# Optimization experiments

Measured on AMD Instinct MI355X. Metric: run time of the kernel, lower is better.

## Reference

```python
import jax, jax.numpy as jnp
import numpy as np

TEMPERATURE = 0.1
EPS = 1e-12  # F.normalize eps

B, D = 4096, 1024

def setup_inputs() -> dict:
    key = jax.random.key(0)
    k1, k2 = jax.random.split(key)
    return {
        "feature_view_1": jax.random.normal(k1, (B, D), dtype=jnp.float32),
        "feature_view_2": jax.random.normal(k2, (B, D), dtype=jnp.float32),
    }

def reference(feature_view_1, feature_view_2):
    b = feature_view_1.shape[0]
    n = 2 * b  # n_views = 2
    # cat views and L2-normalize each row (F.normalize semantics: x / max(||x||, eps))
    f = jnp.concatenate([feature_view_1, feature_view_2], axis=0)  # [2B, D]
    norm = jnp.maximum(jnp.linalg.norm(f, axis=1, keepdims=True), EPS)
    f = f / norm
    # similarity matrix scaled by temperature
    sim = jnp.matmul(f, f.T) / TEMPERATURE  # [2B, 2B]
    idx = jnp.arange(n)
    # positive for row i is the other view of the same sample: column (i+B) mod 2B
    pos = sim[idx, (idx + b) % n]  # [2B]
    # cross-entropy with label 0 over [pos, negatives] == lse over off-diagonal minus pos
    sim_offdiag = jnp.where(idx[:, None] == idx[None, :], -jnp.inf, sim)
    lse = jax.nn.logsumexp(sim_offdiag, axis=1)  # [2B]
    # CrossEntropyLoss default reduction: mean
    return jnp.mean(lse - pos)
```

## Files before the change

kernel.cpp:

```cpp
#include <hip/hip_runtime.h>
#include <stdint.h>

#define B_ROWS 4096
#define N_ROWS 8192
#define D_DIM  1024
#define NBLK   64
#define NTRI   2080
#define XCDQ   260

typedef __attribute__((ext_vector_type(4))) float f32x4;

static __device__ __forceinline__ void async_copy16(const unsigned char* g, unsigned char* l) {
  __builtin_amdgcn_global_load_lds(
      (const __attribute__((address_space(1))) unsigned int*)g,
      (__attribute__((address_space(3))) unsigned int*)l, 16, 0, 0);
}

static __device__ __forceinline__ void wg_barrier() {
  asm volatile("" ::: "memory");
  __builtin_amdgcn_s_barrier();
  asm volatile("" ::: "memory");
}

__global__ __launch_bounds__(256) void normalize_kernel(
    const float* __restrict__ f1, const float* __restrict__ f2,
    unsigned char* __restrict__ F8, float* __restrict__ rowsum) {
  const int row = blockIdx.x;
  const int tid = threadIdx.x;
  const float* src = (row < B_ROWS) ? (f1 + (size_t)row * D_DIM)
                                    : (f2 + (size_t)(row - B_ROWS) * D_DIM);
  float4 v = ((const float4*)src)[tid];
  float ss = v.x * v.x + v.y * v.y + v.z * v.z + v.w * v.w;
#pragma unroll
  for (int m = 1; m < 64; m <<= 1) ss += __shfl_xor(ss, m, 64);
  __shared__ float red[4];
  if ((tid & 63) == 0) red[tid >> 6] = ss;
  __syncthreads();
  ss = red[0] + red[1] + red[2] + red[3];
  const float s16 = 16.0f / fmaxf(sqrtf(ss), 1e-12f);
  int w = 0;
  w = __builtin_amdgcn_cvt_pk_fp8_f32(v.x * s16, v.y * s16, w, 0);
  w = __builtin_amdgcn_cvt_pk_fp8_f32(v.z * s16, v.w * s16, w, 1);
  ((int*)(F8 + (size_t)row * D_DIM))[tid] = w;
  if (tid == 0) rowsum[row] = 0.0f;
}

__global__ __launch_bounds__(256, 3) void simloss_kernel(
    const unsigned char* __restrict__ F8, float* __restrict__ rowsum,
    float* __restrict__ pos) {
  __shared__ __align__(16) unsigned char lA[3][128 * 64];
  __shared__ __align__(16) unsigned char lB[3][128 * 64];

  int s = (blockIdx.x & 7) * XCDQ + (blockIdx.x >> 3);
  int SJ = 0;
  for (;;) { const int c = 64 * SJ + 36; if (s < c) break; s -= c; ++SJ; }
  int SI = 0;
  while (SI < SJ && s >= 64) { s -= 64; ++SI; }
  int di, dj;
  if (SI < SJ) {
    dj = s >> 3; di = s & 7;
  } else {
    dj = 0; while (s > dj) { s -= (dj + 1); ++dj; } di = s;
  }
  const int bi = SI * 8 + di;
  const int bj = SJ * 8 + dj;

  const int tid  = threadIdx.x;
  const int lane = tid & 63;
  const int wv   = __builtin_amdgcn_readfirstlane(tid >> 6);
  const int waveRow = wv >> 1;
  const int waveCol = wv & 1;
  const int q   = lane >> 4;
  const int l16 = lane & 15;

  const int iBase = bi * 128;
  const int jBase = bj * 128;
  const unsigned char* __restrict__ GA = F8 + (size_t)iBase * D_DIM;
  const unsigned char* __restrict__ GB = F8 + (size_t)jBase * D_DIM;

  f32x4 acc[4][4];
#pragma unroll
  for (int a = 0; a < 4; ++a)
#pragma unroll
    for (int b = 0; b < 4; ++b) acc[a][b] = (f32x4){0.f, 0.f, 0.f, 0.f};

#define STAGE(BUFI, K0)                                                      \
  {                                                                          \
    _Pragma("unroll") for (int it = 0; it < 2; ++it) {                       \
      const int lc = it * 256 + tid;                                         \
      const int rr = lc >> 2;                                                \
      const int gc = (lc & 3) ^ ((rr >> 1) & 3);                             \
      const size_t goff = (size_t)rr * D_DIM + (K0) + gc * 16;               \
      async_copy16(GA + goff, &lA[BUFI][lc * 16]);                           \
    }                                                                        \
    _Pragma("unroll") for (int it = 0; it < 2; ++it) {                       \
      const int lc = it * 256 + tid;                                         \
      const int rr = lc >> 2;                                                \
      const int gc = (lc & 3) ^ ((rr >> 1) & 3);                             \
      const size_t goff = (size_t)rr * D_DIM + (K0) + gc * 16;               \
      async_copy16(GB + goff, &lB[BUFI][lc * 16]);                           \
    }                                                                        \
  }

#define STEP(BUFI)                                                           \
  {                                                                          \
    long aF[4][2], bF[4][2];                                                 \
    _Pragma("unroll") for (int mi = 0; mi < 4; ++mi) {                       \
      const int rr  = waveRow * 64 + mi * 16 + l16;                          \
      const int swz = (rr >> 1) & 3;                                         \
      const int base = rr * 64 + ((q & 1) << 3);                             \
      aF[mi][0] = *(const long*)&lA[BUFI][base + ((((q >> 1)    ) ^ swz) << 4)]; \
      aF[mi][1] = *(const long*)&lA[BUFI][base + ((((q >> 1) + 2) ^ swz) << 4)]; \
    }                                                                        \
    _Pragma("unroll") for (int ni = 0; ni < 4; ++ni) {                       \
      const int rr  = waveCol * 64 + ni * 16 + l16;                          \
      const int swz = (rr >> 1) & 3;                                         \
      const int base = rr * 64 + ((q & 1) << 3);                             \
      bF[ni][0] = *(const long*)&lB[BUFI][base + ((((q >> 1)    ) ^ swz) << 4)]; \
      bF[ni][1] = *(const long*)&lB[BUFI][base + ((((q >> 1) + 2) ^ swz) << 4)]; \
    }                                                                        \
    _Pragma("unroll") for (int mi = 0; mi < 4; ++mi)                         \
      _Pragma("unroll") for (int ni = 0; ni < 4; ++ni) {                     \
        acc[mi][ni] = __builtin_amdgcn_mfma_f32_16x16x32_fp8_fp8(            \
            aF[mi][0], bF[ni][0], acc[mi][ni], 0, 0, 0);                     \
        acc[mi][ni] = __builtin_amdgcn_mfma_f32_16x16x32_fp8_fp8(            \
            aF[mi][1], bF[ni][1], acc[mi][ni], 0, 0, 0);                     \
      }                                                                      \
  }

  STAGE(0, 0)
  STAGE(1, 64)

#pragma unroll 1
  for (int t = 0; t < 16; ++t) {
    if (t == 15) { asm volatile("s_waitcnt vmcnt(0)" ::: "memory"); }
    else         { asm volatile("s_waitcnt vmcnt(4)" ::: "memory"); }
    wg_barrier();
    if (t < 14) { STAGE((t + 2) % 3, (t + 2) * 64) }
    STEP(t % 3)
  }
#undef STEP
#undef STAGE

  const bool offdiag = (bi != bj);
  float colAcc[4] = {0.f, 0.f, 0.f, 0.f};

#pragma unroll
  for (int mi = 0; mi < 4; ++mi) {
#pragma unroll
    for (int reg = 0; reg < 4; ++reg) {
      const int i = iBase + waveRow * 64 + mi * 16 + q * 4 + reg;
      float s2 = 0.0f;
#pragma unroll
      for (int ni = 0; ni < 4; ++ni) {
        const int j = jBase + waveCol * 64 + ni * 16 + l16;
        const float sim = acc[mi][ni][reg] * (10.0f / 256.0f);
        const float e = (j == i) ? 0.0f : __expf(sim - 10.0f);
        s2 += e;
        colAcc[ni] += e;
        if (i < B_ROWS && j == i + B_ROWS) pos[i] = sim;
      }
#pragma unroll
      for (int m = 1; m < 16; m <<= 1) s2 += __shfl_xor(s2, m, 64);
      if (l16 == 0) atomicAdd(&rowsum[i], s2);
    }
  }

  if (offdiag) {
#pragma unroll
    for (int ni = 0; ni < 4; ++ni) {
      float c = colAcc[ni];
      c += __shfl_xor(c, 16, 64);
      c += __shfl_xor(c, 32, 64);
      if (q == 0) {
        const int j = jBase + waveCol * 64 + ni * 16 + l16;
        atomicAdd(&rowsum[j], c);
      }
    }
  }
}

__global__ __launch_bounds__(1024) void finalize_kernel(
    const float* __restrict__ rowsum, const float* __restrict__ pos,
    float* __restrict__ out) {
  const int tid = threadIdx.x;
  float a = 0.0f;
  for (int i = tid; i < N_ROWS; i += 1024)
    a += logf(rowsum[i]) + 10.0f - pos[i & (B_ROWS - 1)];
#pragma unroll
  for (int m = 1; m < 64; m <<= 1) a += __shfl_xor(a, m, 64);
  __shared__ float red[16];
  if ((tid & 63) == 0) red[tid >> 6] = a;
  __syncthreads();
  if (tid == 0) {
    float t = 0.0f;
#pragma unroll
    for (int w = 0; w < 16; ++w) t += red[w];
    out[0] = t * (1.0f / N_ROWS);
  }
}

extern "C" void kernel_launch(void* const* d_in, const int* in_sizes, int n_in,
                              void* d_out, int out_size, void* d_ws, size_t ws_size,
                              hipStream_t stream) {
  const float* f1 = (const float*)d_in[0];
  const float* f2 = (const float*)d_in[1];
  unsigned char* F8 = (unsigned char*)d_ws;
  float* rowsum = (float*)((char*)d_ws + (size_t)N_ROWS * D_DIM);
  float* pos    = rowsum + N_ROWS;
  float* out    = (float*)d_out;

  hipLaunchKernelGGL(normalize_kernel, dim3(N_ROWS), dim3(256), 0, stream, f1, f2, F8, rowsum);
  hipLaunchKernelGGL(simloss_kernel, dim3(NTRI), dim3(256), 0, stream, F8, rowsum, pos);
  hipLaunchKernelGGL(finalize_kernel, dim3(1), dim3(1024), 0, stream, rowsum, pos, out);
}
```

Measured before the change: 150.4 us.

## Switch FP8 GEMM to 32x32x64 scaled MFMA with matching LDS swizzle

Replaces the 16x16x32 FP8 MFMA tiling (4x4 tiles per wave, two MFMAs per k-step) with the gfx950 32x32x64 f8f6f4 scaled MFMA (2x2 tiles per wave, one MFMA per k-step) using unit scales. The LDS swizzle and fragment loads change to 16-byte vector reads per half-wave, and the epilogue is remapped to the 32x32 accumulator layout. This is meant to cut MFMA issue count and LDS read instructions, at the cost of wider shuffle reductions in the epilogue and reliance on the new layout mapping being correct.

```diff
diff --git a/kernel.cpp b/kernel.cpp
--- a/kernel.cpp
+++ b/kernel.cpp
@@ -8,7 +8,9 @@
 #define NTRI   2080
 #define XCDQ   260
 
-typedef __attribute__((ext_vector_type(4))) float f32x4;
+typedef __attribute__((ext_vector_type(4)))  int   i32x4;
+typedef __attribute__((ext_vector_type(8)))  int   i32x8;
+typedef __attribute__((ext_vector_type(16))) float f32x16;
 
 static __device__ __forceinline__ void async_copy16(const unsigned char* g, unsigned char* l) {
   __builtin_amdgcn_global_load_lds(
@@ -70,33 +72,33 @@
   const int wv   = __builtin_amdgcn_readfirstlane(tid >> 6);
   const int waveRow = wv >> 1;
   const int waveCol = wv & 1;
-  const int q   = lane >> 4;
-  const int l16 = lane & 15;
+  const int l31 = lane & 31;
+  const int h   = lane >> 5;
 
   const int iBase = bi * 128;
   const int jBase = bj * 128;
   const unsigned char* __restrict__ GA = F8 + (size_t)iBase * D_DIM;
   const unsigned char* __restrict__ GB = F8 + (size_t)jBase * D_DIM;
 
-  f32x4 acc[4][4];
-#pragma unroll
-  for (int a = 0; a < 4; ++a)
-#pragma unroll
-    for (int b = 0; b < 4; ++b) acc[a][b] = (f32x4){0.f, 0.f, 0.f, 0.f};
+  f32x16 acc[2][2];
+#pragma unroll
+  for (int a = 0; a < 2; ++a)
+#pragma unroll
+    for (int b = 0; b < 2; ++b) acc[a][b] = (f32x16)(0.0f);
 
 #define STAGE(BUFI, K0)                                                      \
   {                                                                          \
     _Pragma("unroll") for (int it = 0; it < 2; ++it) {                       \
       const int lc = it * 256 + tid;                                         \
       const int rr = lc >> 2;                                                \
-      const int gc = (lc & 3) ^ ((rr >> 1) & 3);                             \
+      const int gc = (lc & 3) ^ (rr & 3);                                    \
       const size_t goff = (size_t)rr * D_DIM + (K0) + gc * 16;               \
       async_copy16(GA + goff, &lA[BUFI][lc * 16]);                           \
     }                                                                        \
     _Pragma("unroll") for (int it = 0; it < 2; ++it) {                       \
       const int lc = it * 256 + tid;                                         \
       const int rr = lc >> 2;                                                \
-      const int gc = (lc & 3) ^ ((rr >> 1) & 3);                             \
+      const int gc = (lc & 3) ^ (rr & 3);                                    \
       const size_t goff = (size_t)rr * D_DIM + (K0) + gc * 16;               \
       async_copy16(GB + goff, &lB[BUFI][lc * 16]);                           \
     }                                                                        \
@@ -104,28 +106,25 @@
 
 #define STEP(BUFI)                                                           \
   {                                                                          \
-    long aF[4][2], bF[4][2];                                                 \
-    _Pragma("unroll") for (int mi = 0; mi < 4; ++mi) {                       \
-      const int rr  = waveRow * 64 + mi * 16 + l16;                          \
-      const int swz = (rr >> 1) & 3;                                         \
-      const int base = rr * 64 + ((q & 1) << 3);                             \
-      aF[mi][0] = *(const long*)&lA[BUFI][base + ((((q >> 1)    ) ^ swz) << 4)]; \
-      aF[mi][1] = *(const long*)&lA[BUFI][base + ((((q >> 1) + 2) ^ swz) << 4)]; \
-    }                                                                        \
-    _Pragma("unroll") for (int ni = 0; ni < 4; ++ni) {                       \
-      const int rr  = waveCol * 64 + ni * 16 + l16;                          \
-      const int swz = (rr >> 1) & 3;                                         \
-      const int base = rr * 64 + ((q & 1) << 3);                             \
-      bF[ni][0] = *(const long*)&lB[BUFI][base + ((((q >> 1)    ) ^ swz) << 4)]; \
-      bF[ni][1] = *(const long*)&lB[BUFI][base + ((((q >> 1) + 2) ^ swz) << 4)]; \
-    }                                                                        \
-    _Pragma("unroll") for (int mi = 0; mi < 4; ++mi)                         \
-      _Pragma("unroll") for (int ni = 0; ni < 4; ++ni) {                     \
-        acc[mi][ni] = __builtin_amdgcn_mfma_f32_16x16x32_fp8_fp8(            \
-            aF[mi][0], bF[ni][0], acc[mi][ni], 0, 0, 0);                     \
-        acc[mi][ni] = __builtin_amdgcn_mfma_f32_16x16x32_fp8_fp8(            \
-            aF[mi][1], bF[ni][1], acc[mi][ni], 0, 0, 0);                     \
-      }                                                                      \
+    i32x8 aF[2], bF[2];                                                      \
+    _Pragma("unroll") for (int mi = 0; mi < 2; ++mi) {                       \
+      const int rr = waveRow * 64 + mi * 32 + l31;                           \
+      const int sw = rr & 3;                                                 \
+      const i32x4 lo = *(const i32x4*)&lA[BUFI][(rr * 4 + ((2 * h)     ^ sw)) * 16]; \
+      const i32x4 hi = *(const i32x4*)&lA[BUFI][(rr * 4 + ((2 * h + 1) ^ sw)) * 16]; \
+      aF[mi] = __builtin_shufflevector(lo, hi, 0, 1, 2, 3, 4, 5, 6, 7);      \
+    }                                                                        \
+    _Pragma("unroll") for (int ni = 0; ni < 2; ++ni) {                       \
+      const int rr = waveCol * 64 + ni * 32 + l31;                           \
+      const int sw = rr & 3;                                                 \
+      const i32x4 lo = *(const i32x4*)&lB[BUFI][(rr * 4 + ((2 * h)     ^ sw)) * 16]; \
+      const i32x4 hi = *(const i32x4*)&lB[BUFI][(rr * 4 + ((2 * h + 1) ^ sw)) * 16]; \
+      bF[ni] = __builtin_shufflevector(lo, hi, 0, 1, 2, 3, 4, 5, 6, 7);      \
+    }                                                                        \
+    _Pragma("unroll") for (int mi = 0; mi < 2; ++mi)                         \
+      _Pragma("unroll") for (int ni = 0; ni < 2; ++ni)                       \
+        acc[mi][ni] = __builtin_amdgcn_mfma_scale_f32_32x32x64_f8f6f4(       \
+            aF[mi], bF[ni], acc[mi][ni], 0, 0, 0, 127, 0, 127);              \
   }
 
   STAGE(0, 0)
@@ -143,17 +142,18 @@
 #undef STAGE
 
   const bool offdiag = (bi != bj);
-  float colAcc[4] = {0.f, 0.f, 0.f, 0.f};
-
-#pragma unroll
-  for (int mi = 0; mi < 4; ++mi) {
-#pragma unroll
-    for (int reg = 0; reg < 4; ++reg) {
-      const int i = iBase + waveRow * 64 + mi * 16 + q * 4 + reg;
+  float colAcc[2] = {0.f, 0.f};
+
+#pragma unroll
+  for (int mi = 0; mi < 2; ++mi) {
+#pragma unroll
+    for (int reg = 0; reg < 16; ++reg) {
+      const int i = iBase + waveRow * 64 + mi * 32 +
+                    (reg & 3) + ((reg >> 2) << 3) + (h << 2);
       float s2 = 0.0f;
 #pragma unroll
-      for (int ni = 0; ni < 4; ++ni) {
-        const int j = jBase + waveCol * 64 + ni * 16 + l16;
+      for (int ni = 0; ni < 2; ++ni) {
+        const int j = jBase + waveCol * 64 + ni * 32 + l31;
         const float sim = acc[mi][ni][reg] * (10.0f / 256.0f);
         const float e = (j == i) ? 0.0f : __expf(sim - 10.0f);
         s2 += e;
@@ -161,19 +161,18 @@
         if (i < B_ROWS && j == i + B_ROWS) pos[i] = sim;
       }
 #pragma unroll
-      for (int m = 1; m < 16; m <<= 1) s2 += __shfl_xor(s2, m, 64);
-      if (l16 == 0) atomicAdd(&rowsum[i], s2);
+      for (int m = 1; m < 32; m <<= 1) s2 += __shfl_xor(s2, m, 64);
+      if (l31 == 0) atomicAdd(&rowsum[i], s2);
     }
   }
 
   if (offdiag) {
 #pragma unroll
-    for (int ni = 0; ni < 4; ++ni) {
+    for (int ni = 0; ni < 2; ++ni) {
       float c = colAcc[ni];
-      c += __shfl_xor(c, 16, 64);
       c += __shfl_xor(c, 32, 64);
-      if (q == 0) {
-        const int j = jBase + waveCol * 64 + ni * 16 + l16;
+      if (h == 0) {
+        const int j = jBase + waveCol * 64 + ni * 32 + l31;
         atomicAdd(&rowsum[j], c);
       }
     }
```

New measurement: 156.4 us. +4.0%, slower.
